# Kernel optimization log

Hardware: AMD Instinct MI355X
Metric: run time of the kernel (lower is better)

The kernel has to match this reference:

```python
import jax, jax.numpy as jnp
import numpy as np

B, NV, H, W = 4, 1, 224, 224
GH = GW = 16                 # 224 // 14 patch grid
NT = 1 + GH * GW             # 257 tokens (cls + patches)
CIN, DF, DH = 1152, 512, 128
NP0 = 512
UPF = (4, 8)
RADIUS = 1.0


def setup_inputs():
    key = jax.random.key(0)
    ks = jax.random.split(key, 8)
    rn = lambda k, s, sc: jax.random.normal(k, s) * sc
    points = jax.random.uniform(ks[0], (B, NP0, 3), minval=-0.5, maxval=0.5)
    tokens = rn(ks[1], (B, CIN, NT), 0.5)
    # OpenGL-style c2w (the forward flips cols 1:3 to OpenCV); camera at z=+2 looking at origin
    c2w = np.tile(np.eye(4, dtype=np.float32), (B, NV, 1, 1))
    c2w[..., 2, 3] = 2.0
    K = np.zeros((B, NV, 3, 3), dtype=np.float32)
    K[..., 0, 0] = 250.0; K[..., 1, 1] = 250.0
    K[..., 0, 2] = W / 2.0; K[..., 1, 2] = H / 2.0
    K[..., 2, 2] = 1.0
    return dict(
        points=points, input_image_tokens=tokens,
        c2w_cond=jnp.asarray(c2w), intrinsic_cond=jnp.asarray(K),
        w1=rn(ks[2], (2 * DF, CIN), CIN ** -0.5), b1=jnp.zeros((2 * DF,)),
        w2=rn(ks[3], (DF, 2 * DF), (2 * DF) ** -0.5), b2=jnp.zeros((DF,)),
        s0_w1=rn(ks[4], (DH, 3 + DF), (3 + DF) ** -0.5), s0_b1=jnp.zeros((DH,)),
        s0_ow=rn(ks[5], (UPF[0] * 3, DH), DH ** -0.5), s0_ob=jnp.zeros((UPF[0] * 3,)),
        s1_w1=rn(ks[6], (DH, 3 + DF), (3 + DF) ** -0.5), s1_b1=jnp.zeros((DH,)),
        s1_ow=rn(ks[7], (UPF[1] * 3, DH), DH ** -0.5), s1_ob=jnp.zeros((UPF[1] * 3,)))


def _points_projection(pts, c2w, K, lf):
    # pts: (B,N,3), c2w: (B,4,4) OpenCV, K: (B,3,3), lf: (B,C,H,W)
    N = pts.shape[1]
    w2c = jnp.linalg.inv(c2w)
    cam = jnp.einsum('bij,bnj->bni', w2c[:, :3, :3], pts) + w2c[:, None, :3, 3]
    z = cam[..., 2]
    zs = jnp.where(jnp.abs(z) > 1e-8, z, 1e-8)
    px = K[:, 0, 0][:, None] * cam[..., 0] / zs + K[:, 0, 2][:, None]
    py = K[:, 1, 1][:, None] * cam[..., 1] / zs + K[:, 1, 2][:, None]
    ix = jnp.floor(px).astype(jnp.int32)
    iy = jnp.floor(py).astype(jnp.int32)
    valid = (z > 1e-6) & (ix >= 0) & (ix < W) & (iy >= 0) & (iy < H)
    pix = jnp.where(valid, iy * W + ix, H * W)                  # (B,N); dummy bin H*W
    nseg = B * (H * W + 1)
    seg = (jnp.arange(B)[:, None] * (H * W + 1) + pix).reshape(-1)
    zf = jnp.where(valid, z, jnp.inf).reshape(-1)
    minz = jax.ops.segment_min(zf, seg, num_segments=nseg)      # z-buffer (points_per_pixel=1)
    ismin = valid.reshape(-1) & (zf <= minz[seg])
    pid = jnp.arange(B * N)
    win = jax.ops.segment_min(jnp.where(ismin, pid, B * N), seg, num_segments=nseg)
    visible = (pid == win[seg]).reshape(B, N)                   # unique winner per pixel
    lff = lf.reshape(B, -1, H * W)
    g = jnp.take_along_axis(lff, jnp.clip(pix, 0, H * W - 1)[:, None, :], axis=2)  # (B,C,N)
    return jnp.where(visible[:, None, :], g, 0.0)


def reference(points, input_image_tokens, c2w_cond, intrinsic_cond,
              w1, b1, w2, b2, s0_w1, s0_b1, s0_ow, s0_ob, s1_w1, s1_b1, s1_ow, s1_ob):
    # mlp_feat_cond: 1x1 conv MLP over tokens
    feat = jax.nn.relu(jnp.einsum('oc,bcn->bon', w1, input_image_tokens) + b1[:, None])
    feat = jnp.einsum('oc,bcn->bon', w2, feat) + b2[:, None]    # (B, DF, NT)
    # OpenGL -> OpenCV flip of c2w columns 1:3
    flip = jnp.ones((4, 4)).at[:3, 1:3].set(-1.0)
    c2w = c2w_cond[:, 0] * flip
    Kmat = intrinsic_cond[:, 0]
    # drop cls token, to patch grid, bilinear upsample to image resolution
    lf = jnp.transpose(feat, (0, 2, 1))[:, 1:].reshape(B, GH, GW, DF)
    lf = jnp.transpose(lf, (0, 3, 1, 2))
    lf = jax.image.resize(lf, (B, DF, H, W), method='bilinear')  # (B, DF, H, W)
    pts = points
    pcd = jnp.transpose(points, (0, 2, 1))                      # (B,3,N)
    stages = (((s0_w1, s0_b1, s0_ow, s0_ob), UPF[0]), ((s1_w1, s1_b1, s1_ow, s1_ob), UPF[1]))
    outs = []
    for (ws, bs, ow, ob), f in stages:
        up_cond = _points_projection(pts, c2w, Kmat, lf)        # (B, DF, N) visibility-masked gather
        h = jax.nn.relu(jnp.einsum('oc,bcn->bon', ws,
                                   jnp.concatenate([pcd, up_cond], axis=1)) + bs[:, None])
        off = jnp.tanh(jnp.einsum('oc,bcn->bon', ow, h) + ob[:, None])  # (B, 3f, N)
        n = pcd.shape[2]
        off = off.reshape(B, f, 3, n).transpose(0, 2, 3, 1).reshape(B, 3, n * f)
        pcd = jnp.repeat(pcd, f, axis=2) + off * RADIUS         # SPD-style bounded upsample
        pts = jnp.transpose(pcd, (0, 2, 1))
        outs.append(pts)
    return tuple(outs)
```

## Files before the change

kernel.cpp:

```cpp
#include <hip/hip_runtime.h>
#include <hip/hip_bf16.h>
#include <cstdint>
#include <cstddef>

using bf16 = __hip_bfloat16;
typedef __attribute__((ext_vector_type(8))) short bf16x8_t;
typedef __attribute__((ext_vector_type(4))) float f32x4_t;

#define BB 4
#define HH 224
#define WWD 224
#define NTOK 257
#define CINC 1152
#define DFC 512

constexpr size_t OFF_G2    = 256;
constexpr size_t OFF_WC    = OFF_G2;
constexpr size_t OFF_T     = OFF_G2 + 1052672;
constexpr size_t OFF_SCR   = 256 + 2105344;
constexpr size_t OFF_FEAT1 = OFF_SCR;
constexpr size_t OFF_ZBUF  = OFF_SCR;
constexpr size_t OFF_PINFO = OFF_SCR + 1605632;
constexpr size_t WS_NEED   = OFF_SCR + 1736704;
constexpr size_t WS_FULL   = OFF_SCR + 4210688;

__device__ __forceinline__ float ldf(const void* p, size_t i, bool f32) {
  return f32 ? ((const float*)p)[i] : __bfloat162float(((const bf16*)p)[i]);
}
__device__ __forceinline__ double ldd(const void* p, size_t i, bool f32) {
  return f32 ? (double)((const float*)p)[i]
             : (double)__bfloat162float(((const bf16*)p)[i]);
}
__device__ __forceinline__ bool detect_f32(const void* c2w_raw) {
  const float* fc = (const float*)c2w_raw;
  return (fc[0] == 1.0f) && (fc[5] == 1.0f);
}

__device__ void compute_cam(const void* c2w_raw, const void* K_raw, int b, bool f32,
                            double* cw) {
  double m[16];
#pragma unroll
  for (int i = 0; i < 16; ++i) m[i] = ldd(c2w_raw, b*16 + i, f32);
  m[1]=-m[1]; m[2]=-m[2]; m[5]=-m[5]; m[6]=-m[6]; m[9]=-m[9]; m[10]=-m[10];
  double i0  =  m[5]*m[10]*m[15] - m[5]*m[11]*m[14] - m[9]*m[6]*m[15] + m[9]*m[7]*m[14] + m[13]*m[6]*m[11] - m[13]*m[7]*m[10];
  double i4  = -m[4]*m[10]*m[15] + m[4]*m[11]*m[14] + m[8]*m[6]*m[15] - m[8]*m[7]*m[14] - m[12]*m[6]*m[11] + m[12]*m[7]*m[10];
  double i8  =  m[4]*m[9]*m[15]  - m[4]*m[11]*m[13] - m[8]*m[5]*m[15] + m[8]*m[7]*m[13] + m[12]*m[5]*m[11] - m[12]*m[7]*m[9];
  double i12 = -m[4]*m[9]*m[14]  + m[4]*m[10]*m[13] + m[8]*m[5]*m[14] - m[8]*m[6]*m[13] - m[12]*m[5]*m[10] + m[12]*m[6]*m[9];
  double i1  = -m[1]*m[10]*m[15] + m[1]*m[11]*m[14] + m[9]*m[2]*m[15] - m[9]*m[3]*m[14] - m[13]*m[2]*m[11] + m[13]*m[3]*m[10];
  double i5  =  m[0]*m[10]*m[15] - m[0]*m[11]*m[14] - m[8]*m[2]*m[15] + m[8]*m[3]*m[14] + m[12]*m[2]*m[11] - m[12]*m[3]*m[10];
  double i9  = -m[0]*m[9]*m[15]  + m[0]*m[11]*m[13] + m[8]*m[1]*m[15] - m[8]*m[3]*m[13] - m[12]*m[1]*m[11] + m[12]*m[3]*m[9];
  double i13 =  m[0]*m[9]*m[14]  - m[0]*m[10]*m[13] - m[8]*m[1]*m[14] + m[8]*m[2]*m[13] + m[12]*m[1]*m[10] - m[12]*m[2]*m[9];
  double i2  =  m[1]*m[6]*m[15]  - m[1]*m[7]*m[14]  - m[5]*m[2]*m[15] + m[5]*m[3]*m[14] + m[13]*m[2]*m[7]  - m[13]*m[3]*m[6];
  double i6  = -m[0]*m[6]*m[15]  + m[0]*m[7]*m[14]  + m[4]*m[2]*m[15] - m[4]*m[3]*m[14] - m[12]*m[2]*m[7]  + m[12]*m[3]*m[6];
  double i10 =  m[0]*m[5]*m[15]  - m[0]*m[7]*m[13]  - m[4]*m[1]*m[15] + m[4]*m[3]*m[13] + m[12]*m[1]*m[7]  - m[12]*m[3]*m[5];
  double i14 = -m[0]*m[5]*m[14]  + m[0]*m[6]*m[13]  + m[4]*m[1]*m[14] - m[4]*m[2]*m[13] - m[12]*m[1]*m[6]  + m[12]*m[2]*m[5];
  double i3  = -m[1]*m[6]*m[11]  + m[1]*m[7]*m[10]  + m[5]*m[2]*m[11] - m[5]*m[3]*m[10] - m[9]*m[2]*m[7]   + m[9]*m[3]*m[6];
  double i7  =  m[0]*m[6]*m[11]  - m[0]*m[7]*m[10]  - m[4]*m[2]*m[11] + m[4]*m[3]*m[10] + m[8]*m[2]*m[7]   - m[8]*m[3]*m[6];
  double i11 = -m[0]*m[5]*m[11]  + m[0]*m[7]*m[9]   + m[4]*m[1]*m[11] - m[4]*m[3]*m[9]  - m[8]*m[1]*m[7]   + m[8]*m[3]*m[5];
  double det = m[0]*i0 + m[1]*i4 + m[2]*i8 + m[3]*i12;
  double r = 1.0 / det;
  cw[0]=i0*r;  cw[1]=i1*r;  cw[2]=i2*r;  cw[3]=i3*r;
  cw[4]=i4*r;  cw[5]=i5*r;  cw[6]=i6*r;  cw[7]=i7*r;
  cw[8]=i8*r;  cw[9]=i9*r;  cw[10]=i10*r; cw[11]=i11*r;
  cw[12] = ldd(K_raw, b*9+0, f32);
  cw[13] = ldd(K_raw, b*9+2, f32);
  cw[14] = ldd(K_raw, b*9+4, f32);
  cw[15] = ldd(K_raw, b*9+5, f32);
}

template <int XK, int WK, bool TROUT, bool ATOMIC, bool BSTR, int PREC>
__global__ __launch_bounds__(256) void gemm_mfma(
    const void* __restrict__ Wm, const void* __restrict__ Wm2,
    const void* __restrict__ X, const void* __restrict__ xb,
    const float* __restrict__ bstr_p, int bstr,
    float* __restrict__ Y, const void* __restrict__ c2w_raw,
    int O, int K, int Nn, int Yld,
    int bx0, int bxm, int by0, int bym,
    int Wld, int Wc0, int skn) {
  __shared__ __align__(16) short SMEM[6 * 2560];
  short* Whi = SMEM;
  short* Wmd = SMEM + 2560;
  short* Wlo = SMEM + 5120;
  short* Xhi = SMEM + 7680;
  short* Xmd = SMEM + 10240;
  short* Xlo = SMEM + 12800;
  const bool f32 = detect_f32(c2w_raw);
  int tid = threadIdx.x;
  int n0 = blockIdx.x * 64;
  int o0 = blockIdx.y * 64;
  int bz = (int)blockIdx.z;
  int bidx = bz / skn;
  int ks = bz - bidx * skn;
  int bx = bx0 + bxm * bidx;
  int by = by0 + bym * bidx;
  int kq = K / skn;
  int kbase = ks * kq;
  int so  = tid >> 2;
  int skq = tid & 3;
  int sn  = tid & 63;
  int skg = tid >> 6;
  int wv = tid >> 6, lane = tid & 63;
  int lm = lane & 15, lq = lane >> 4;

  float wreg[8], xreg[8];
  f32x4_t acc[4] = {};

  auto load_w = [&](int c0) {
    if constexpr (WK == 3) {
      int orow = o0 + so;
      const void* Wp = (orow < 128) ? Wm : Wm2;
      size_t base = (size_t)(orow & 127) * Wld + Wc0 + c0 + skq * 8;
#pragma unroll
      for (int j = 0; j < 8; ++j) wreg[j] = ldf(Wp, base + j, f32);
    } else if constexpr (WK == 1) {
      const float* Wf = (const float*)Wm;
      size_t base = (size_t)(o0 + so) * Wld + c0 + skq * 8;
      float4 v0 = *(const float4*)(Wf + base);
      float4 v1 = *(const float4*)(Wf + base + 4);
      wreg[0]=v0.x; wreg[1]=v0.y; wreg[2]=v0.z; wreg[3]=v0.w;
      wreg[4]=v1.x; wreg[5]=v1.y; wreg[6]=v1.z; wreg[7]=v1.w;
    } else {
      size_t base = (size_t)(o0 + so) * Wld + c0 + skq * 8;
      if (f32) {
        const float* Wf = (const float*)Wm;
        float4 v0 = *(const float4*)(Wf + base);
        float4 v1 = *(const float4*)(Wf + base + 4);
        wreg[0]=v0.x; wreg[1]=v0.y; wreg[2]=v0.z; wreg[3]=v0.w;
        wreg[4]=v1.x; wreg[5]=v1.y; wreg[6]=v1.z; wreg[7]=v1.w;
      } else {
        const unsigned short* Wh = (const unsigned short*)Wm;
        ushort4 u0 = *(const ushort4*)(Wh + base);
        ushort4 u1 = *(const ushort4*)(Wh + base + 4);
        wreg[0]=__uint_as_float((unsigned)u0.x<<16); wreg[1]=__uint_as_float((unsigned)u0.y<<16);
        wreg[2]=__uint_as_float((unsigned)u0.z<<16); wreg[3]=__uint_as_float((unsigned)u0.w<<16);
        wreg[4]=__uint_as_float((unsigned)u1.x<<16); wreg[5]=__uint_as_float((unsigned)u1.y<<16);
        wreg[6]=__uint_as_float((unsigned)u1.z<<16); wreg[7]=__uint_as_float((unsigned)u1.w<<16);
      }
    }
  };
  auto load_x = [&](int c0) {
    int gn = n0 + sn;
#pragma unroll
    for (int j = 0; j < 8; ++j) {
      int c = c0 + skg * 8 + j;
      float v = 0.f;
      if (gn < Nn) {
        if (XK == 3) {
          v = (gn < 1024) ? ldf(X, (size_t)c * 1024 + gn, f32)
                          : ((gn == 1024) ? ldf(xb, c, f32) : 0.f);
        } else if (XK == 2) {
          size_t xi = ((size_t)bx * K + c) * Nn + gn;
          v = fmaxf(((const float*)X)[xi] + ldf(xb, c, f32), 0.f);
        } else {
          size_t xi = ((size_t)bx * K + c) * Nn + gn;
          v = ldf(X, xi, f32);
        }
      }
      xreg[j] = v;
    }
  };
  auto store_hi = [&](const float* r, short* hp, int off) {
    int hd[4];
#pragma unroll
    for (int d = 0; d < 4; ++d) {
      unsigned b0 = __float_as_uint(r[2*d]), b1 = __float_as_uint(r[2*d+1]);
      hd[d] = (int)((b0 >> 16) | (b1 & 0xFFFF0000u));
    }
    *(int4*)&hp[off] = make_int4(hd[0], hd[1], hd[2], hd[3]);
  };
  auto split_store3 = [&](const float* r, short* hp, short* mp, short* lp, int off) {
    int hd[4], md[4], ld[4];
#pragma unroll
    for (int d = 0; d < 4; ++d) {
      float v0 = r[2*d], v1 = r[2*d+1];
      unsigned b0 = __float_as_uint(v0), b1 = __float_as_uint(v1);
      hd[d] = (int)((b0 >> 16) | (b1 & 0xFFFF0000u));
      float h0 = __uint_as_float(b0 & 0xFFFF0000u);
      float h1 = __uint_as_float(b1 & 0xFFFF0000u);
      float r0 = v0 - h0, r1 = v1 - h1;
      unsigned c0 = __float_as_uint(r0), c1 = __float_as_uint(r1);
      md[d] = (int)((c0 >> 16) | (c1 & 0xFFFF0000u));
      float m0 = __uint_as_float(c0 & 0xFFFF0000u);
      float m1 = __uint_as_float(c1 & 0xFFFF0000u);
      unsigned e0 = __float_as_uint(r0 - m0), e1 = __float_as_uint(r1 - m1);
      ld[d] = (int)((e0 >> 16) | (e1 & 0xFFFF0000u));
    }
    *(int4*)&hp[off] = make_int4(hd[0], hd[1], hd[2], hd[3]);
    *(int4*)&mp[off] = make_int4(md[0], md[1], md[2], md[3]);
    *(int4*)&lp[off] = make_int4(ld[0], ld[1], ld[2], ld[3]);
  };

  int nkt = kq / 32;
  int woff = so * 40 + skq * 8;
  int xoff = sn * 40 + skg * 8;
  int aoff = (wv * 16 + lm) * 40 + lq * 8;
  load_w(kbase); load_x(kbase);

  if (PREC == 0 && !f32) {
    for (int kt = 0; kt < nkt; ++kt) {
      __syncthreads();
      store_hi(wreg, Whi, woff);
      store_hi(xreg, Xhi, xoff);
      __syncthreads();
      if (kt + 1 < nkt) { load_w(kbase + (kt + 1) * 32); load_x(kbase + (kt + 1) * 32); }
      bf16x8_t ahi = *(const bf16x8_t*)&Whi[aoff];
#pragma unroll
      for (int nt = 0; nt < 4; ++nt) {
        int boff = (nt * 16 + lm) * 40 + lq * 8;
        bf16x8_t bhi = *(const bf16x8_t*)&Xhi[boff];
        acc[nt] = __builtin_amdgcn_mfma_f32_16x16x32_bf16(ahi, bhi, acc[nt], 0, 0, 0);
      }
    }
  } else {
    for (int kt = 0; kt < nkt; ++kt) {
      __syncthreads();
      split_store3(wreg, Whi, Wmd, Wlo, woff);
      split_store3(xreg, Xhi, Xmd, Xlo, xoff);
      __syncthreads();
      if (kt + 1 < nkt) { load_w(kbase + (kt + 1) * 32); load_x(kbase + (kt + 1) * 32); }
      bf16x8_t ahi = *(const bf16x8_t*)&Whi[aoff];
      bf16x8_t amd = *(const bf16x8_t*)&Wmd[aoff];
      bf16x8_t alo = *(const bf16x8_t*)&Wlo[aoff];
#pragma unroll
      for (int nt = 0; nt < 4; ++nt) {
        int boff = (nt * 16 + lm) * 40 + lq * 8;
        bf16x8_t bhi = *(const bf16x8_t*)&Xhi[boff];
        bf16x8_t bmd = *(const bf16x8_t*)&Xmd[boff];
        bf16x8_t blo = *(const bf16x8_t*)&Xlo[boff];
        acc[nt] = __builtin_amdgcn_mfma_f32_16x16x32_bf16(ahi, blo, acc[nt], 0, 0, 0);
        acc[nt] = __builtin_amdgcn_mfma_f32_16x16x32_bf16(amd, bmd, acc[nt], 0, 0, 0);
        acc[nt] = __builtin_amdgcn_mfma_f32_16x16x32_bf16(alo, bhi, acc[nt], 0, 0, 0);
        acc[nt] = __builtin_amdgcn_mfma_f32_16x16x32_bf16(amd, bhi, acc[nt], 0, 0, 0);
        acc[nt] = __builtin_amdgcn_mfma_f32_16x16x32_bf16(ahi, bmd, acc[nt], 0, 0, 0);
        acc[nt] = __builtin_amdgcn_mfma_f32_16x16x32_bf16(ahi, bhi, acc[nt], 0, 0, 0);
      }
    }
  }

  if (!ATOMIC) {
#pragma unroll
    for (int nt = 0; nt < 4; ++nt) {
      int gn = n0 + nt * 16 + lm;
      if (gn < Nn) {
#pragma unroll
        for (int r = 0; r < 4; ++r) {
          int o = o0 + wv * 16 + lq * 4 + r;
          size_t yi = TROUT ? ((size_t)by * Nn + gn) * Yld + o
                            : ((size_t)by * O + o) * (size_t)Yld + gn;
          Y[yi] = acc[nt][r];
        }
      }
    }
  } else if (!TROUT) {
#pragma unroll
    for (int nt = 0; nt < 4; ++nt) {
      int gn = n0 + nt * 16 + lm;
      if (gn < Nn) {
#pragma unroll
        for (int r = 0; r < 4; ++r) {
          int o = o0 + wv * 16 + lq * 4 + r;
          float v = acc[nt][r];
          if (BSTR && ks == 0) v += bstr_p[(size_t)o * bstr];
          atomicAdd(&Y[((size_t)by * O + o) * (size_t)Yld + gn], v);
        }
      }
    }
  } else {
    __syncthreads();
    float* ts = (float*)SMEM;
#pragma unroll
    for (int nt = 0; nt < 4; ++nt) {
      int n = nt * 16 + lm;
      int ob = wv * 16 + lq * 4;
#pragma unroll
      for (int r = 0; r < 4; ++r) ts[(ob + r) * 65 + n] = acc[nt][r];
    }
    __syncthreads();
    int oo = tid & 63;
    int nb = tid >> 6;
    float bv = (BSTR && ks == 0) ? bstr_p[(size_t)(o0 + oo) * bstr] : 0.f;
#pragma unroll
    for (int i = 0; i < 16; ++i) {
      int n = nb * 16 + i;
      int gn = n0 + n;
      if (gn < Nn)
        atomicAdd(&Y[((size_t)by * Nn + gn) * (size_t)Yld + o0 + oo],
                  ts[oo * 65 + n] + bv);
    }
  }
}

template <int XK, bool RELU, bool TROUT>
__global__ __launch_bounds__(256) void gemm_k(const void* __restrict__ Wm, const void* __restrict__ X,
                                              const void* __restrict__ bias, float* __restrict__ Y,
                                              const void* __restrict__ c2w_raw, int O, int K, int Nn,
                                              int bx0, int bxm, int by0, int bym) {
  const int TK = 32;
  __shared__ __align__(16) float Ws[TK * 68];
  __shared__ __align__(16) float Xs[TK * 68];
  const bool f32 = detect_f32(c2w_raw);
  int tid = threadIdx.x;
  int n0 = blockIdx.x * 64;
  int o0 = blockIdx.y * 64;
  int bx = bx0 + bxm * (int)blockIdx.z;
  int by = by0 + bym * (int)blockIdx.z;
  int tx = tid & 15, ty = tid >> 4;
  int wo  = tid >> 3;
  int wk4 = tid & 7;
  float acc[4][4] = {};
  float4 wv[2];
  float  xv[8];

  auto load_tile = [&](int c0) {
#pragma unroll
    for (int i = 0; i < 2; ++i) {
      int o = wo + i * 32;
      size_t off = (size_t)(o0 + o) * K + c0 + 4 * wk4;
      if (f32) {
        wv[i] = *(const float4*)((const float*)Wm + off);
      } else {
        ushort4 u = *(const ushort4*)((const unsigned short*)Wm + off);
        wv[i] = make_float4(__uint_as_float((unsigned)u.x << 16),
                            __uint_as_float((unsigned)u.y << 16),
                            __uint_as_float((unsigned)u.z << 16),
                            __uint_as_float((unsigned)u.w << 16));
      }
    }
#pragma unroll
    for (int i = 0; i < 8; ++i) {
      int idx = i * 256 + tid;
      int n = idx & 63, k = idx >> 6;
      int gn = n0 + n;
      float v = 0.f;
      if (gn < Nn) {
        size_t xi = ((size_t)bx * K + c0 + k) * Nn + gn;
        v = (XK == 0) ? ldf(X, xi, f32) : ((const float*)X)[xi];
      }
      xv[i] = v;
    }
  };

  int nkt = K / TK;
  load_tile(0);
  for (int kt = 0; kt < nkt; ++kt) {
    __syncthreads();
#pragma unroll
    for (int i = 0; i < 2; ++i) {
      int o = wo + i * 32;
      Ws[(4 * wk4 + 0) * 68 + o] = wv[i].x;
      Ws[(4 * wk4 + 1) * 68 + o] = wv[i].y;
      Ws[(4 * wk4 + 2) * 68 + o] = wv[i].z;
      Ws[(4 * wk4 + 3) * 68 + o] = wv[i].w;
    }
#pragma unroll
    for (int i = 0; i < 8; ++i) {
      int idx = i * 256 + tid;
      int n = idx & 63, k = idx >> 6;
      Xs[k * 68 + n] = xv[i];
    }
    __syncthreads();
    if (kt + 1 < nkt) load_tile((kt + 1) * TK);
#pragma unroll
    for (int k = 0; k < TK; ++k) {
      const float4 a  = *(const float4*)&Ws[k * 68 + tx * 4];
      const float4 bb = *(const float4*)&Xs[k * 68 + ty * 4];
      acc[0][0] = fmaf(a.x, bb.x, acc[0][0]); acc[0][1] = fmaf(a.x, bb.y, acc[0][1]);
      acc[0][2] = fmaf(a.x, bb.z, acc[0][2]); acc[0][3] = fmaf(a.x, bb.w, acc[0][3]);
      acc[1][0] = fmaf(a.y, bb.x, acc[1][0]); acc[1][1] = fmaf(a.y, bb.y, acc[1][1]);
      acc[1][2] = fmaf(a.y, bb.z, acc[1][2]); acc[1][3] = fmaf(a.y, bb.w, acc[1][3]);
      acc[2][0] = fmaf(a.z, bb.x, acc[2][0]); acc[2][1] = fmaf(a.z, bb.y, acc[2][1]);
      acc[2][2] = fmaf(a.z, bb.z, acc[2][2]); acc[2][3] = fmaf(a.z, bb.w, acc[2][3]);
      acc[3][0] = fmaf(a.w, bb.x, acc[3][0]); acc[3][1] = fmaf(a.w, bb.y, acc[3][1]);
      acc[3][2] = fmaf(a.w, bb.z, acc[3][2]); acc[3][3] = fmaf(a.w, bb.w, acc[3][3]);
    }
  }
#pragma unroll
  for (int oi = 0; oi < 4; ++oi) {
    int o = o0 + tx * 4 + oi;
    float bv = ldf(bias, o, f32);
#pragma unroll
    for (int ni = 0; ni < 4; ++ni) {
      int gn = n0 + ty * 4 + ni;
      if (gn < Nn) {
        float v = acc[oi][ni] + bv;
        if (RELU) v = fmaxf(v, 0.f);
        size_t yi = TROUT ? ((size_t)by * Nn + gn) * O + o
                          : ((size_t)by * O + o) * Nn + gn;
        Y[yi] = v;
      }
    }
  }
}

template <int PMODE>
__global__ __launch_bounds__(256) void proj_k(const void* __restrict__ pts,
                                              const void* __restrict__ c2w_raw,
                                              const void* __restrict__ K_raw,
                                              unsigned long long* __restrict__ zbuf,
                                              int* __restrict__ pinfo, int N) {
  int m = blockIdx.x * 256 + threadIdx.x;
  if (m >= BB * N) return;
  const bool f32 = detect_f32(c2w_raw);
  int b = m / N;
  double cw[16];
  compute_cam(c2w_raw, K_raw, b, f32, cw);
  double px, py, pz;
  if (PMODE == 1) {
    const float* pf = (const float*)pts;
    px = pf[m*3+0]; py = pf[m*3+1]; pz = pf[m*3+2];
  } else {
    px = ldd(pts, (size_t)m*3+0, f32);
    py = ldd(pts, (size_t)m*3+1, f32);
    pz = ldd(pts, (size_t)m*3+2, f32);
  }
  double cx = cw[0]*px + cw[1]*py + cw[2]*pz + cw[3];
  double cy = cw[4]*px + cw[5]*py + cw[6]*pz + cw[7];
  double z  = cw[8]*px + cw[9]*py + cw[10]*pz + cw[11];
  double zs = (fabs(z) > 1e-8) ? z : 1e-8;
  double fpx = cw[12] * cx / zs + cw[13];
  double fpy = cw[14] * cy / zs + cw[15];
  double fix = floor(fpx), fiy = floor(fpy);
  bool valid = (z > 1e-6) && (fix >= 0.0) && (fix < (double)WWD) && (fiy >= 0.0) && (fiy < (double)HH);
  int* pi = pinfo + (size_t)m * 4;
  if (valid) {
    int ix = (int)fix, iy = (int)fiy;
    int zidx = b * (HH * WWD) + iy * WWD + ix;
    float zf = (float)z;
    unsigned long long key = ((unsigned long long)__float_as_uint(zf) << 32) | (unsigned)m;
    atomicMin(&zbuf[zidx], key);
    pi[0] = zidx; pi[1] = 1;
    *(unsigned long long*)(pi + 2) = key;
  } else {
    pi[0] = 0; pi[1] = 0; pi[2] = 0; pi[3] = 0;
  }
}

template <int PMODE, int F, int TM>
__global__ __launch_bounds__(256) void stage2_k(
    const void* __restrict__ pts_in,
    const float* __restrict__ Tm,
    const int* __restrict__ pinfo,
    const unsigned long long* __restrict__ zbuf,
    const void* __restrict__ w1,
    const void* __restrict__ b1,
    const void* __restrict__ ow,
    const void* __restrict__ ob,
    const void* __restrict__ c2w_raw,
    float* __restrict__ out,
    int N) {
  constexpr int TPP = 256 / TM;
  constexpr int OC  = 128 / TPP;
  __shared__ int   ro_s[TM * 4];
  __shared__ float wt_s[TM * 4];
  __shared__ float p_s[TM * 3];
  __shared__ float Wp_s[128 * 3];
  __shared__ float b1_s[128];
  __shared__ __align__(16) float ow_s[F * 3 * 132];
  __shared__ __align__(16) float Hs[TM * 132];

  const bool f32 = detect_f32(c2w_raw);
  int tid = threadIdx.x;
  int m0 = blockIdx.x * TM;

  if (tid < TM) {
    int m = m0 + tid;
    const int* pi = pinfo + (size_t)m * 4;
    int zidx = pi[0];
    unsigned long long key = *(const unsigned long long*)(pi + 2);
    bool vis = pi[1] && (zbuf[zidx] == key);
    float s = vis ? 1.f : 0.f;
    int b = m / N;
    int rem = zidx - b * (HH * WWD);
    int iy = rem / WWD, ix = rem - iy * WWD;
    float sx = fminf(fmaxf(((float)ix + 0.5f) / 14.0f - 0.5f, 0.f), 15.f);
    float sy = fminf(fmaxf(((float)iy + 0.5f) / 14.0f - 0.5f, 0.f), 15.f);
    int x0 = (int)sx, y0 = (int)sy;
    int x1 = min(x0 + 1, 15), y1 = min(y0 + 1, 15);
    float fx = sx - (float)x0, fy = sy - (float)y0;
    int base = b * NTOK;
    ro_s[tid*4+0] = (base + 1 + y0*16 + x0) * 256;
    ro_s[tid*4+1] = (base + 1 + y0*16 + x1) * 256;
    ro_s[tid*4+2] = (base + 1 + y1*16 + x0) * 256;
    ro_s[tid*4+3] = (base + 1 + y1*16 + x1) * 256;
    wt_s[tid*4+0] = s * (1.f-fy)*(1.f-fx);
    wt_s[tid*4+1] = s * (1.f-fy)*fx;
    wt_s[tid*4+2] = s * fy*(1.f-fx);
    wt_s[tid*4+3] = s * fy*fx;
#pragma unroll
    for (int d = 0; d < 3; ++d) {
      p_s[tid*3 + d] = (PMODE == 1) ? ((const float*)pts_in)[(size_t)m*3 + d]
                                    : ldf(pts_in, (size_t)m*3 + d, f32);
    }
  }
  for (int i = tid; i < 128 * 3; i += 256) Wp_s[i] = ldf(w1, (size_t)(i / 3) * 515 + (i % 3), f32);
  for (int i = tid; i < 128; i += 256) b1_s[i] = ldf(b1, i, f32);
  for (int i = tid; i < F * 3 * 128; i += 256) ow_s[(i >> 7) * 132 + (i & 127)] = ldf(ow, i, f32);
  __syncthreads();

  {
    int pt = tid / TPP;
    int tx = tid % TPP;
    int oc0 = tx * OC;
    const float* t0p = Tm + ro_s[pt*4+0] + oc0;
    const float* t1p = Tm + ro_s[pt*4+1] + oc0;
    const float* t2p = Tm + ro_s[pt*4+2] + oc0;
    const float* t3p = Tm + ro_s[pt*4+3] + oc0;
    float w0 = wt_s[pt*4+0], w1v = wt_s[pt*4+1], w2v = wt_s[pt*4+2], w3v = wt_s[pt*4+3];
    float px = p_s[pt*3+0], py = p_s[pt*3+1], pz = p_s[pt*3+2];
#pragma unroll
    for (int i = 0; i < OC; i += 4) {
      f32x4_t c0 = *(const f32x4_t*)(t0p + i);
      f32x4_t c1 = *(const f32x4_t*)(t1p + i);
      f32x4_t c2 = *(const f32x4_t*)(t2p + i);
      f32x4_t c3 = *(const f32x4_t*)(t3p + i);
      f32x4_t hv;
#pragma unroll
      for (int j = 0; j < 4; ++j) {
        int o = oc0 + i + j;
        float v = b1_s[o]
                + Wp_s[o*3+0]*px + Wp_s[o*3+1]*py + Wp_s[o*3+2]*pz
                + w0*c0[j] + w1v*c1[j] + w2v*c2[j] + w3v*c3[j];
        hv[j] = fmaxf(v, 0.f);
      }
      *(f32x4_t*)&Hs[pt * 132 + oc0 + i] = hv;
    }
  }
  __syncthreads();

  const int tasks = TM * F * 3;
  for (int t = tid; t < tasks; t += 256) {
    int mI = t % TM;
    int r  = t / TM;
    f32x4_t acc4 = {0.f, 0.f, 0.f, 0.f};
#pragma unroll
    for (int k = 0; k < 128; k += 4) {
      f32x4_t hv = *(const f32x4_t*)&Hs[mI * 132 + k];
      f32x4_t wv = *(const f32x4_t*)&ow_s[r * 132 + k];
      acc4 += hv * wv;
    }
    float dot = acc4[0] + acc4[1] + acc4[2] + acc4[3] + ldf(ob, r, f32);
    float val = tanhf(dot);
    int j = r / 3, d = r - j * 3;
    int m = m0 + mI;
    out[((size_t)m * F + j) * 3 + d] = p_s[mI * 3 + d] + val;
  }
}

template <int PMODE, int F>
__global__ __launch_bounds__(256) void stage_k(
    const void* __restrict__ pts_in,
    const float* __restrict__ g2,
    const int* __restrict__ pinfo,
    const unsigned long long* __restrict__ zbuf,
    const void* __restrict__ w1,
    const void* __restrict__ b1,
    const void* __restrict__ ow,
    const void* __restrict__ ob,
    const void* __restrict__ c2w_raw,
    float* __restrict__ out,
    int N) {
  const int TM = 16, TK = 32;
  __shared__ int   ro_s[TM * 4];
  __shared__ float wt_s[TM * 4];
  __shared__ float p_s[TM * 3];
  __shared__ float ow_s[F * 3 * 128];
  __shared__ __align__(16) float uni[4800];
  float* Ws = uni;
  float* Vs = uni + 4224;
  float* Hs = uni;

  const bool f32 = detect_f32(c2w_raw);
  int tid = threadIdx.x;
  int m0 = blockIdx.x * TM;

  if (tid < TM) {
    int m = m0 + tid;
    const int* pi = pinfo + (size_t)m * 4;
    int zidx = pi[0];
    unsigned long long key = *(const unsigned long long*)(pi + 2);
    bool vis = pi[1] && (zbuf[zidx] == key);
    float s = vis ? 1.f : 0.f;
    int b = m / N;
    int rem = zidx - b * (HH * WWD);
    int iy = rem / WWD, ix = rem - iy * WWD;
    float sx = fminf(fmaxf(((float)ix + 0.5f) / 14.0f - 0.5f, 0.f), 15.f);
    float sy = fminf(fmaxf(((float)iy + 0.5f) / 14.0f - 0.5f, 0.f), 15.f);
    int x0 = (int)sx, y0 = (int)sy;
    int x1 = min(x0 + 1, 15), y1 = min(y0 + 1, 15);
    float fx = sx - (float)x0, fy = sy - (float)y0;
    int base = b * NTOK;
    ro_s[tid*4+0] = (base + 1 + y0*16 + x0) * DFC;
    ro_s[tid*4+1] = (base + 1 + y0*16 + x1) * DFC;
    ro_s[tid*4+2] = (base + 1 + y1*16 + x0) * DFC;
    ro_s[tid*4+3] = (base + 1 + y1*16 + x1) * DFC;
    wt_s[tid*4+0] = s * (1.f-fy)*(1.f-fx);
    wt_s[tid*4+1] = s * (1.f-fy)*fx;
    wt_s[tid*4+2] = s * fy*(1.f-fx);
    wt_s[tid*4+3] = s * fy*fx;
#pragma unroll
    for (int d = 0; d < 3; ++d) {
      p_s[tid*3 + d] = (PMODE == 1) ? ((const float*)pts_in)[(size_t)m*3 + d]
                                    : ldf(pts_in, (size_t)m*3 + d, f32);
    }
  }
  for (int i = tid; i < F * 3 * 128; i += 256) ow_s[i] = ldf(ow, i, f32);
  __syncthreads();

  int tx = tid & 15, ty = tid >> 4;
  float acc[2][4] = {};
  float wreg[16];
  float greg[2][4];
  float vbase[2];

  auto prefetch = [&](int c0) {
    if (f32) {
      const float* w1f = (const float*)w1;
#pragma unroll
      for (int i = 0; i < 16; ++i) {
        int idx = i * 256 + tid;
        int k = idx & 31, o = idx >> 5;
        int c = c0 + k;
        wreg[i] = (c < 515) ? w1f[(size_t)o * 515 + c] : 0.f;
      }
    } else {
      const bf16* w1h = (const bf16*)w1;
#pragma unroll
      for (int i = 0; i < 16; ++i) {
        int idx = i * 256 + tid;
        int k = idx & 31, o = idx >> 5;
        int c = c0 + k;
        wreg[i] = (c < 515) ? __bfloat162float(w1h[(size_t)o * 515 + c]) : 0.f;
      }
    }
#pragma unroll
    for (int i = 0; i < 2; ++i) {
      int idx = i * 256 + tid;
      int mI = idx & 15, k = idx >> 4;
      int c = c0 + k;
      vbase[i] = 0.f;
      greg[i][0] = greg[i][1] = greg[i][2] = greg[i][3] = 0.f;
      if (c < 3) {
        vbase[i] = p_s[mI*3 + c];
      } else if (c < 515) {
        int ch = c - 3;
        greg[i][0] = g2[ro_s[mI*4+0] + ch];
        greg[i][1] = g2[ro_s[mI*4+1] + ch];
        greg[i][2] = g2[ro_s[mI*4+2] + ch];
        greg[i][3] = g2[ro_s[mI*4+3] + ch];
      }
    }
  };

  prefetch(0);
  for (int kt = 0; kt < 17; ++kt) {
    __syncthreads();
#pragma unroll
    for (int i = 0; i < 16; ++i) {
      int idx = i * 256 + tid;
      int k = idx & 31, o = idx >> 5;
      Ws[k * 132 + o] = wreg[i];
    }
#pragma unroll
    for (int i = 0; i < 2; ++i) {
      int idx = i * 256 + tid;
      int mI = idx & 15, k = idx >> 4;
      Vs[k * 18 + mI] = vbase[i]
        + wt_s[mI*4+0] * greg[i][0] + wt_s[mI*4+1] * greg[i][1]
        + wt_s[mI*4+2] * greg[i][2] + wt_s[mI*4+3] * greg[i][3];
    }
    __syncthreads();
    if (kt + 1 < 17) prefetch((kt + 1) * TK);
#pragma unroll
    for (int k = 0; k < TK; ++k) {
      const float4 a0 = *(const float4*)&Ws[k * 132 + tx * 4];
      const float4 a1 = *(const float4*)&Ws[k * 132 + 64 + tx * 4];
      const float  bb = Vs[k * 18 + ty];
      acc[0][0] = fmaf(a0.x, bb, acc[0][0]);
      acc[0][1] = fmaf(a0.y, bb, acc[0][1]);
      acc[0][2] = fmaf(a0.z, bb, acc[0][2]);
      acc[0][3] = fmaf(a0.w, bb, acc[0][3]);
      acc[1][0] = fmaf(a1.x, bb, acc[1][0]);
      acc[1][1] = fmaf(a1.y, bb, acc[1][1]);
      acc[1][2] = fmaf(a1.z, bb, acc[1][2]);
      acc[1][3] = fmaf(a1.w, bb, acc[1][3]);
    }
  }
  __syncthreads();
#pragma unroll
  for (int h = 0; h < 2; ++h) {
#pragma unroll
    for (int oi = 0; oi < 4; ++oi) {
      int o = h * 64 + tx * 4 + oi;
      float bv = ldf(b1, o, f32);
      Hs[o * 18 + ty] = fmaxf(acc[h][oi] + bv, 0.f);
    }
  }
  __syncthreads();
  const int tasks = TM * F * 3;
  for (int t = tid; t < tasks; t += 256) {
    int mI = t & 15, r = t >> 4;
    float dot = ldf(ob, r, f32);
#pragma unroll 8
    for (int k = 0; k < 128; ++k) dot = fmaf(ow_s[r * 128 + k], Hs[k * 18 + mI], dot);
    float val = tanhf(dot);
    int j = r / 3, d = r - j * 3;
    int m = m0 + mI;
    out[((size_t)m * F + j) * 3 + d] = p_s[mI * 3 + d] + val;
  }
}

extern "C" void kernel_launch(void* const* d_in, const int* in_sizes, int n_in,
                              void* d_out, int out_size, void* d_ws, size_t ws_size,
                              hipStream_t stream) {
  const void* points = d_in[0];
  const void* tokens = d_in[1];
  const void* c2w    = d_in[2];
  const void* intr   = d_in[3];
  const void* w1     = d_in[4];
  const void* b1     = d_in[5];
  const void* w2     = d_in[6];
  const void* b2     = d_in[7];
  const void* s0w1   = d_in[8];
  const void* s0b1   = d_in[9];
  const void* s0ow   = d_in[10];
  const void* s0ob   = d_in[11];
  const void* s1w1   = d_in[12];
  const void* s1b1   = d_in[13];
  const void* s1ow   = d_in[14];
  const void* s1ob   = d_in[15];

  if (ws_size < WS_NEED) {
    hipMemsetAsync(d_out, 0, (size_t)out_size * sizeof(float), stream);
    return;
  }

  char* ws = (char*)d_ws;
  unsigned long long* zbuf = (unsigned long long*)(ws + OFF_ZBUF);
  int* pinfo    = (int*)(ws + OFF_PINFO);
  float* out    = (float*)d_out;
  float* out0   = out;
  float* out1   = out + 24576;

  const int NB = (NTOK + 63) / 64;
  const size_t zbytes = (size_t)BB * HH * WWD * 8;

  if (ws_size >= WS_FULL) {
    float* Wc    = (float*)(ws + OFF_WC);
    float* Tb    = (float*)(ws + OFF_T);
    float* feat1 = (float*)(ws + OFF_FEAT1);

    hipMemsetAsync(ws + OFF_WC, 0, 2105344, stream);
    hipMemsetAsync(feat1, 0, 4210688, stream);

    gemm_mfma<3, 3, false, true, false, 0><<<dim3(17, 4, 4), 256, 0, stream>>>(
        s0w1, s1w1, w2, b2, nullptr, 0, Wc, c2w,
        256, 512, 1025, 1028, 0, 0, 0, 0, 515, 3, 4);

    gemm_mfma<0, 0, false, true, false, 0><<<dim3(NB, 16, 12), 256, 0, stream>>>(
        w1, nullptr, tokens, nullptr, nullptr, 0, feat1, c2w,
        1024, CINC, NTOK, NTOK, 0, 1, 0, 1, CINC, 0, 3);

    gemm_mfma<2, 1, true, true, true, 1><<<dim3(NB, 4, 32), 256, 0, stream>>>(
        Wc, nullptr, feat1, b1, Wc + 1024, 1028, Tb, c2w,
        256, 1024, NTOK, 256, 0, 1, 0, 1, 1028, 0, 8);

    hipMemsetAsync(zbuf, 0xFF, zbytes, stream);
    proj_k<0><<<(BB * 512) / 256, 256, 0, stream>>>(points, c2w, intr, zbuf, pinfo, 512);
    stage2_k<0, 4, 8><<<(BB * 512) / 8, 256, 0, stream>>>(points, Tb, pinfo, zbuf,
                                                          s0w1, s0b1, s0ow, s0ob, c2w,
                                                          out0, 512);
    hipMemsetAsync(zbuf, 0xFF, zbytes, stream);
    proj_k<1><<<(BB * 2048) / 256, 256, 0, stream>>>(out0, c2w, intr, zbuf, pinfo, 2048);
    stage2_k<1, 8, 8><<<(BB * 2048) / 8, 256, 0, stream>>>(out0, Tb + 128, pinfo, zbuf,
                                                           s1w1, s1b1, s1ow, s1ob, c2w,
                                                           out1, 2048);
  } else {
    float* g2    = (float*)(ws + OFF_G2);
    float* feat1 = (float*)(ws + OFF_FEAT1);
    for (int b = 0; b < BB; ++b) {
      gemm_k<0, true, false><<<dim3(NB, 16, 1), 256, 0, stream>>>(
          w1, tokens, b1, feat1, c2w, 1024, CINC, NTOK, b, 0, 0, 0);
      gemm_k<1, false, true><<<dim3(NB, 8, 1), 256, 0, stream>>>(
          w2, feat1, b2, g2, c2w, 512, 1024, NTOK, 0, 0, b, 0);
    }
    hipMemsetAsync(zbuf, 0xFF, zbytes, stream);
    proj_k<0><<<(BB * 512) / 256, 256, 0, stream>>>(points, c2w, intr, zbuf, pinfo, 512);
    stage_k<0, 4><<<(BB * 512) / 16, 256, 0, stream>>>(points, g2, pinfo, zbuf,
                                                       s0w1, s0b1, s0ow, s0ob, c2w,
                                                       out0, 512);
    hipMemsetAsync(zbuf, 0xFF, zbytes, stream);
    proj_k<1><<<(BB * 2048) / 256, 256, 0, stream>>>(out0, c2w, intr, zbuf, pinfo, 2048);
    stage_k<1, 8><<<(BB * 2048) / 16, 256, 0, stream>>>(out0, g2, pinfo, zbuf,
                                                        s1w1, s1b1, s1ow, s1ob, c2w,
                                                        out1, 2048);
  }
}
```

Measured before the change: 218.0 us.

## Restructure pipeline: split-K partials, fp32 second GEMM, fused stage-1 projection

The first GEMM now writes split-K partial sums to separate buffers instead of using atomics, and it skips the cls token. A new fp32 SIMT GEMM sums those partials, adds the bias and applies ReLU while loading, then computes the second projection. Stage 0 now projects its own output points into a second z-buffer, which removes a separate projection kernel. Both z-buffers are cleared with a single memset, and the feat1 memset is dropped. In exchange the workspace grows much larger, the full path is taken only when the workspace is big enough, and the second GEMM moves off MFMA to plain FMA.

```diff
diff --git a/kernel.cpp b/kernel.cpp
--- a/kernel.cpp
+++ b/kernel.cpp
@@ -14,15 +14,18 @@
 #define CINC 1152
 #define DFC 512
 
-constexpr size_t OFF_G2    = 256;
-constexpr size_t OFF_WC    = OFF_G2;
-constexpr size_t OFF_T     = OFF_G2 + 1052672;
-constexpr size_t OFF_SCR   = 256 + 2105344;
-constexpr size_t OFF_FEAT1 = OFF_SCR;
-constexpr size_t OFF_ZBUF  = OFF_SCR;
-constexpr size_t OFF_PINFO = OFF_SCR + 1605632;
-constexpr size_t WS_NEED   = OFF_SCR + 1736704;
-constexpr size_t WS_FULL   = OFF_SCR + 4210688;
+constexpr size_t OFF_WC     = 256;
+constexpr size_t OFF_T      = OFF_WC + 1052672;
+constexpr size_t OFF_FP     = OFF_T + 1048576;
+constexpr size_t OFF_ZB0    = OFF_FP + 12582912;
+constexpr size_t OFF_ZB1    = OFF_ZB0 + 1605632;
+constexpr size_t OFF_PI0    = OFF_ZB1 + 1605632;
+constexpr size_t OFF_PI1    = OFF_PI0 + 32768;
+constexpr size_t WS_FULL4   = OFF_PI1 + 131072;
+constexpr size_t OFF_SCR    = 256 + 2105344;
+constexpr size_t OFF_ZBUF   = OFF_SCR;
+constexpr size_t OFF_PINFO  = OFF_SCR + 1605632;
+constexpr size_t WS_NEED    = OFF_SCR + 1736704;
 
 __device__ __forceinline__ float ldf(const void* p, size_t i, bool f32) {
   return f32 ? ((const float*)p)[i] : __bfloat162float(((const bf16*)p)[i]);
@@ -68,13 +71,38 @@
   cw[15] = ldd(K_raw, b*9+5, f32);
 }
 
-template <int XK, int WK, bool TROUT, bool ATOMIC, bool BSTR, int PREC>
+__device__ __forceinline__ void project_point(
+    double px, double py, double pz, const double* cw, int b, int m,
+    unsigned long long* __restrict__ zbuf, int* __restrict__ pinfo) {
+  double cx = cw[0]*px + cw[1]*py + cw[2]*pz + cw[3];
+  double cy = cw[4]*px + cw[5]*py + cw[6]*pz + cw[7];
+  double z  = cw[8]*px + cw[9]*py + cw[10]*pz + cw[11];
+  double zs = (fabs(z) > 1e-8) ? z : 1e-8;
+  double fpx = cw[12] * cx / zs + cw[13];
+  double fpy = cw[14] * cy / zs + cw[15];
+  double fix = floor(fpx), fiy = floor(fpy);
+  bool valid = (z > 1e-6) && (fix >= 0.0) && (fix < (double)WWD) && (fiy >= 0.0) && (fiy < (double)HH);
+  int* pi = pinfo + (size_t)m * 4;
+  if (valid) {
+    int ix = (int)fix, iy = (int)fiy;
+    int zidx = b * (HH * WWD) + iy * WWD + ix;
+    float zf = (float)z;
+    unsigned long long key = ((unsigned long long)__float_as_uint(zf) << 32) | (unsigned)m;
+    atomicMin(&zbuf[zidx], key);
+    pi[0] = zidx; pi[1] = 1;
+    *(unsigned long long*)(pi + 2) = key;
+  } else {
+    pi[0] = 0; pi[1] = 0; pi[2] = 0; pi[3] = 0;
+  }
+}
+
+template <int XK, int WK, bool TROUT, bool ATOMIC, bool BSTR, int PREC, bool PART = false>
 __global__ __launch_bounds__(256) void gemm_mfma(
     const void* __restrict__ Wm, const void* __restrict__ Wm2,
     const void* __restrict__ X, const void* __restrict__ xb,
     const float* __restrict__ bstr_p, int bstr,
     float* __restrict__ Y, const void* __restrict__ c2w_raw,
-    int O, int K, int Nn, int Yld,
+    int O, int K, int Nn, int Yld, int Xld, int Xc0,
     int bx0, int bxm, int by0, int bym,
     int Wld, int Wc0, int skn) {
   __shared__ __align__(16) short SMEM[6 * 2560];
@@ -112,13 +140,6 @@
       size_t base = (size_t)(orow & 127) * Wld + Wc0 + c0 + skq * 8;
 #pragma unroll
       for (int j = 0; j < 8; ++j) wreg[j] = ldf(Wp, base + j, f32);
-    } else if constexpr (WK == 1) {
-      const float* Wf = (const float*)Wm;
-      size_t base = (size_t)(o0 + so) * Wld + c0 + skq * 8;
-      float4 v0 = *(const float4*)(Wf + base);
-      float4 v1 = *(const float4*)(Wf + base + 4);
-      wreg[0]=v0.x; wreg[1]=v0.y; wreg[2]=v0.z; wreg[3]=v0.w;
-      wreg[4]=v1.x; wreg[5]=v1.y; wreg[6]=v1.z; wreg[7]=v1.w;
     } else {
       size_t base = (size_t)(o0 + so) * Wld + c0 + skq * 8;
       if (f32) {
@@ -148,11 +169,8 @@
         if (XK == 3) {
           v = (gn < 1024) ? ldf(X, (size_t)c * 1024 + gn, f32)
                           : ((gn == 1024) ? ldf(xb, c, f32) : 0.f);
-        } else if (XK == 2) {
-          size_t xi = ((size_t)bx * K + c) * Nn + gn;
-          v = fmaxf(((const float*)X)[xi] + ldf(xb, c, f32), 0.f);
         } else {
-          size_t xi = ((size_t)bx * K + c) * Nn + gn;
+          size_t xi = ((size_t)bx * K + c) * Xld + Xc0 + gn;
           v = ldf(X, xi, f32);
         }
       }
@@ -237,7 +255,20 @@
     }
   }
 
-  if (!ATOMIC) {
+  if constexpr (PART) {
+    float* Yp = Y + (size_t)ks * (size_t)bstr;
+#pragma unroll
+    for (int nt = 0; nt < 4; ++nt) {
+      int gn = n0 + nt * 16 + lm;
+      if (gn < Nn) {
+#pragma unroll
+        for (int r = 0; r < 4; ++r) {
+          int o = o0 + wv * 16 + lq * 4 + r;
+          Yp[((size_t)by * O + o) * (size_t)Yld + gn] = acc[nt][r];
+        }
+      }
+    }
+  } else if (!ATOMIC) {
 #pragma unroll
     for (int nt = 0; nt < 4; ++nt) {
       int gn = n0 + nt * 16 + lm;
@@ -251,7 +282,7 @@
         }
       }
     }
-  } else if (!TROUT) {
+  } else {
 #pragma unroll
     for (int nt = 0; nt < 4; ++nt) {
       int gn = n0 + nt * 16 + lm;
@@ -265,28 +296,101 @@
         }
       }
     }
-  } else {
+  }
+}
+
+template <int SK>
+__global__ __launch_bounds__(256) void tgemm_k(
+    const float* __restrict__ Wc,
+    const float* __restrict__ fp,
+    const void* __restrict__ b1,
+    float* __restrict__ T,
+    const void* __restrict__ c2w_raw) {
+  const int TK = 32;
+  const int PS = BB * 1024 * 256;
+  __shared__ __align__(16) float uni[64 * 68];
+  float* Ws = uni;
+  float* Xs = uni + TK * 68;
+  const bool f32 = detect_f32(c2w_raw);
+  int tid = threadIdx.x;
+  int n0 = blockIdx.x * 64;
+  int o0 = blockIdx.y * 64;
+  int bz = (int)blockIdx.z;
+  int b  = bz / SK;
+  int ks = bz - b * SK;
+  const int kq = 1024 / SK;
+  int kbase = ks * kq;
+  int tx = tid & 15, ty = tid >> 4;
+  int wo = tid >> 3, wk4 = tid & 7;
+  float acc[4][4] = {};
+  float4 wv[2];
+  float xv[8];
+
+  auto load_tile = [&](int c0) {
+#pragma unroll
+    for (int i = 0; i < 2; ++i) {
+      int o = o0 + wo + i * 32;
+      wv[i] = *(const float4*)(Wc + (size_t)o * 1028 + kbase + c0 + 4 * wk4);
+    }
+#pragma unroll
+    for (int i = 0; i < 8; ++i) {
+      int idx = i * 256 + tid;
+      int n = idx & 63, k = idx >> 6;
+      int kk = kbase + c0 + k;
+      size_t xi = ((size_t)b * 1024 + kk) * 256 + n0 + n;
+      float v = fp[xi] + fp[PS + xi] + fp[2 * PS + xi] + ldf(b1, kk, f32);
+      xv[i] = fmaxf(v, 0.f);
+    }
+  };
+
+  int nkt = kq / TK;
+  load_tile(0);
+  for (int kt = 0; kt < nkt; ++kt) {
     __syncthreads();
-    float* ts = (float*)SMEM;
-#pragma unroll
-    for (int nt = 0; nt < 4; ++nt) {
-      int n = nt * 16 + lm;
-      int ob = wv * 16 + lq * 4;
-#pragma unroll
-      for (int r = 0; r < 4; ++r) ts[(ob + r) * 65 + n] = acc[nt][r];
+#pragma unroll
+    for (int i = 0; i < 2; ++i) {
+      int o = wo + i * 32;
+      Ws[(4 * wk4 + 0) * 68 + o] = wv[i].x;
+      Ws[(4 * wk4 + 1) * 68 + o] = wv[i].y;
+      Ws[(4 * wk4 + 2) * 68 + o] = wv[i].z;
+      Ws[(4 * wk4 + 3) * 68 + o] = wv[i].w;
+    }
+#pragma unroll
+    for (int i = 0; i < 8; ++i) {
+      int idx = i * 256 + tid;
+      int n = idx & 63, k = idx >> 6;
+      Xs[k * 68 + n] = xv[i];
     }
     __syncthreads();
-    int oo = tid & 63;
-    int nb = tid >> 6;
-    float bv = (BSTR && ks == 0) ? bstr_p[(size_t)(o0 + oo) * bstr] : 0.f;
-#pragma unroll
-    for (int i = 0; i < 16; ++i) {
-      int n = nb * 16 + i;
-      int gn = n0 + n;
-      if (gn < Nn)
-        atomicAdd(&Y[((size_t)by * Nn + gn) * (size_t)Yld + o0 + oo],
-                  ts[oo * 65 + n] + bv);
-    }
+    if (kt + 1 < nkt) load_tile((kt + 1) * TK);
+#pragma unroll
+    for (int k = 0; k < TK; ++k) {
+      const float4 a  = *(const float4*)&Ws[k * 68 + tx * 4];
+      const float4 bb = *(const float4*)&Xs[k * 68 + ty * 4];
+      acc[0][0] = fmaf(a.x, bb.x, acc[0][0]); acc[0][1] = fmaf(a.x, bb.y, acc[0][1]);
+      acc[0][2] = fmaf(a.x, bb.z, acc[0][2]); acc[0][3] = fmaf(a.x, bb.w, acc[0][3]);
+      acc[1][0] = fmaf(a.y, bb.x, acc[1][0]); acc[1][1] = fmaf(a.y, bb.y, acc[1][1]);
+      acc[1][2] = fmaf(a.y, bb.z, acc[1][2]); acc[1][3] = fmaf(a.y, bb.w, acc[1][3]);
+      acc[2][0] = fmaf(a.z, bb.x, acc[2][0]); acc[2][1] = fmaf(a.z, bb.y, acc[2][1]);
+      acc[2][2] = fmaf(a.z, bb.z, acc[2][2]); acc[2][3] = fmaf(a.z, bb.w, acc[2][3]);
+      acc[3][0] = fmaf(a.w, bb.x, acc[3][0]); acc[3][1] = fmaf(a.w, bb.y, acc[3][1]);
+      acc[3][2] = fmaf(a.w, bb.z, acc[3][2]); acc[3][3] = fmaf(a.w, bb.w, acc[3][3]);
+    }
+  }
+  __syncthreads();
+  float* ts = uni;
+#pragma unroll
+  for (int oi = 0; oi < 4; ++oi)
+#pragma unroll
+    for (int ni = 0; ni < 4; ++ni)
+      ts[(tx * 4 + oi) * 65 + ty * 4 + ni] = acc[oi][ni];
+  __syncthreads();
+  int oo = tid & 63, nb = tid >> 6;
+  float bv = (ks == 0) ? Wc[(size_t)(o0 + oo) * 1028 + 1024] : 0.f;
+#pragma unroll
+  for (int i = 0; i < 16; ++i) {
+    int n = nb * 16 + i;
+    atomicAdd(&T[((size_t)b * 256 + n0 + n) * 256 + o0 + oo], ts[oo * 65 + n] + bv);
   }
 }
 
@@ -413,29 +517,10 @@
     py = ldd(pts, (size_t)m*3+1, f32);
     pz = ldd(pts, (size_t)m*3+2, f32);
   }
-  double cx = cw[0]*px + cw[1]*py + cw[2]*pz + cw[3];
-  double cy = cw[4]*px + cw[5]*py + cw[6]*pz + cw[7];
-  double z  = cw[8]*px + cw[9]*py + cw[10]*pz + cw[11];
-  double zs = (fabs(z) > 1e-8) ? z : 1e-8;
-  double fpx = cw[12] * cx / zs + cw[13];
-  double fpy = cw[14] * cy / zs + cw[15];
-  double fix = floor(fpx), fiy = floor(fpy);
-  bool valid = (z > 1e-6) && (fix >= 0.0) && (fix < (double)WWD) && (fiy >= 0.0) && (fiy < (double)HH);
-  int* pi = pinfo + (size_t)m * 4;
-  if (valid) {
-    int ix = (int)fix, iy = (int)fiy;
-    int zidx = b * (HH * WWD) + iy * WWD + ix;
-    float zf = (float)z;
-    unsigned long long key = ((unsigned long long)__float_as_uint(zf) << 32) | (unsigned)m;
-    atomicMin(&zbuf[zidx], key);
-    pi[0] = zidx; pi[1] = 1;
-    *(unsigned long long*)(pi + 2) = key;
-  } else {
-    pi[0] = 0; pi[1] = 0; pi[2] = 0; pi[3] = 0;
-  }
-}
-
-template <int PMODE, int F, int TM>
+  project_point(px, py, pz, cw, b, m, zbuf, pinfo);
+}
+
+template <int PMODE, int F, int TM, bool PROJ>
 __global__ __launch_bounds__(256) void stage2_k(
     const void* __restrict__ pts_in,
     const float* __restrict__ Tm,
@@ -446,6 +531,9 @@
     const void* __restrict__ ow,
     const void* __restrict__ ob,
     const void* __restrict__ c2w_raw,
+    const void* __restrict__ K_raw,
+    unsigned long long* __restrict__ zb_out,
+    int* __restrict__ pinfo_out,
     float* __restrict__ out,
     int N) {
   constexpr int TPP = 256 / TM;
@@ -455,6 +543,7 @@
   __shared__ float p_s[TM * 3];
   __shared__ float Wp_s[128 * 3];
   __shared__ float b1_s[128];
+  __shared__ float op_s[TM * F * 3];
   __shared__ __align__(16) float ow_s[F * 3 * 132];
   __shared__ __align__(16) float Hs[TM * 132];
 
@@ -477,11 +566,11 @@
     int x0 = (int)sx, y0 = (int)sy;
     int x1 = min(x0 + 1, 15), y1 = min(y0 + 1, 15);
     float fx = sx - (float)x0, fy = sy - (float)y0;
-    int base = b * NTOK;
-    ro_s[tid*4+0] = (base + 1 + y0*16 + x0) * 256;
-    ro_s[tid*4+1] = (base + 1 + y0*16 + x1) * 256;
-    ro_s[tid*4+2] = (base + 1 + y1*16 + x0) * 256;
-    ro_s[tid*4+3] = (base + 1 + y1*16 + x1) * 256;
+    int base = b * 256;
+    ro_s[tid*4+0] = (base + y0*16 + x0) * 256;
+    ro_s[tid*4+1] = (base + y0*16 + x1) * 256;
+    ro_s[tid*4+2] = (base + y1*16 + x0) * 256;
+    ro_s[tid*4+3] = (base + y1*16 + x1) * 256;
     wt_s[tid*4+0] = s * (1.f-fy)*(1.f-fx);
     wt_s[tid*4+1] = s * (1.f-fy)*fx;
     wt_s[tid*4+2] = s * fy*(1.f-fx);
@@ -542,7 +631,23 @@
     float val = tanhf(dot);
     int j = r / 3, d = r - j * 3;
     int m = m0 + mI;
-    out[((size_t)m * F + j) * 3 + d] = p_s[mI * 3 + d] + val;
+    float ov = p_s[mI * 3 + d] + val;
+    out[((size_t)m * F + j) * 3 + d] = ov;
+    if (PROJ) op_s[(mI * F + j) * 3 + d] = ov;
+  }
+
+  if constexpr (PROJ) {
+    __syncthreads();
+    if (tid < TM * F) {
+      int mo = m0 * F + tid;
+      int b = mo / (N * F);
+      double cw[16];
+      compute_cam(c2w_raw, K_raw, b, f32, cw);
+      double px = (double)op_s[tid*3+0];
+      double py = (double)op_s[tid*3+1];
+      double pz = (double)op_s[tid*3+2];
+      project_point(px, py, pz, cw, b, mo, zb_out, pinfo_out);
+    }
   }
 }
 
@@ -735,8 +840,6 @@
   }
 
   char* ws = (char*)d_ws;
-  unsigned long long* zbuf = (unsigned long long*)(ws + OFF_ZBUF);
-  int* pinfo    = (int*)(ws + OFF_PINFO);
   float* out    = (float*)d_out;
   float* out0   = out;
   float* out1   = out + 24576;
@@ -744,39 +847,41 @@
   const int NB = (NTOK + 63) / 64;
   const size_t zbytes = (size_t)BB * HH * WWD * 8;
 
-  if (ws_size >= WS_FULL) {
-    float* Wc    = (float*)(ws + OFF_WC);
-    float* Tb    = (float*)(ws + OFF_T);
-    float* feat1 = (float*)(ws + OFF_FEAT1);
-
-    hipMemsetAsync(ws + OFF_WC, 0, 2105344, stream);
-    hipMemsetAsync(feat1, 0, 4210688, stream);
+  if (ws_size >= WS_FULL4) {
+    float* Wc   = (float*)(ws + OFF_WC);
+    float* Tb   = (float*)(ws + OFF_T);
+    float* fp   = (float*)(ws + OFF_FP);
+    unsigned long long* zb0 = (unsigned long long*)(ws + OFF_ZB0);
+    unsigned long long* zb1 = (unsigned long long*)(ws + OFF_ZB1);
+    int* pinfo0 = (int*)(ws + OFF_PI0);
+    int* pinfo1 = (int*)(ws + OFF_PI1);
+
+    hipMemsetAsync(ws + OFF_WC, 0, 2101248, stream);
+    hipMemsetAsync(ws + OFF_ZB0, 0xFF, 2 * zbytes, stream);
 
     gemm_mfma<3, 3, false, true, false, 0><<<dim3(17, 4, 4), 256, 0, stream>>>(
         s0w1, s1w1, w2, b2, nullptr, 0, Wc, c2w,
-        256, 512, 1025, 1028, 0, 0, 0, 0, 515, 3, 4);
-
-    gemm_mfma<0, 0, false, true, false, 0><<<dim3(NB, 16, 12), 256, 0, stream>>>(
-        w1, nullptr, tokens, nullptr, nullptr, 0, feat1, c2w,
-        1024, CINC, NTOK, NTOK, 0, 1, 0, 1, CINC, 0, 3);
-
-    gemm_mfma<2, 1, true, true, true, 1><<<dim3(NB, 4, 32), 256, 0, stream>>>(
-        Wc, nullptr, feat1, b1, Wc + 1024, 1028, Tb, c2w,
-        256, 1024, NTOK, 256, 0, 1, 0, 1, 1028, 0, 8);
-
-    hipMemsetAsync(zbuf, 0xFF, zbytes, stream);
-    proj_k<0><<<(BB * 512) / 256, 256, 0, stream>>>(points, c2w, intr, zbuf, pinfo, 512);
-    stage2_k<0, 4, 8><<<(BB * 512) / 8, 256, 0, stream>>>(points, Tb, pinfo, zbuf,
-                                                          s0w1, s0b1, s0ow, s0ob, c2w,
-                                                          out0, 512);
-    hipMemsetAsync(zbuf, 0xFF, zbytes, stream);
-    proj_k<1><<<(BB * 2048) / 256, 256, 0, stream>>>(out0, c2w, intr, zbuf, pinfo, 2048);
-    stage2_k<1, 8, 8><<<(BB * 2048) / 8, 256, 0, stream>>>(out0, Tb + 128, pinfo, zbuf,
-                                                           s1w1, s1b1, s1ow, s1ob, c2w,
-                                                           out1, 2048);
+        256, 512, 1025, 1028, 1025, 0, 0, 0, 0, 0, 515, 3, 4);
+
+    gemm_mfma<0, 0, false, false, false, 0, true><<<dim3(4, 16, 12), 256, 0, stream>>>(
+        w1, nullptr, tokens, nullptr, nullptr,  1048576, fp, c2w,
+        1024, CINC, 256, 256, 257, 1, 0, 1, 0, 1, CINC, 0, 3);
+
+    proj_k<0><<<(BB * 512) / 256, 256, 0, stream>>>(points, c2w, intr, zb0, pinfo0, 512);
+
+    tgemm_k<4><<<dim3(4, 4, 16), 256, 0, stream>>>(Wc, fp, b1, Tb, c2w);
+
+    stage2_k<0, 4, 8, true><<<(BB * 512) / 8, 256, 0, stream>>>(
+        points, Tb, pinfo0, zb0, s0w1, s0b1, s0ow, s0ob, c2w, intr,
+        zb1, pinfo1, out0, 512);
+    stage2_k<1, 8, 8, false><<<(BB * 2048) / 8, 256, 0, stream>>>(
+        out0, Tb + 128, pinfo1, zb1, s1w1, s1b1, s1ow, s1ob, c2w, intr,
+        nullptr, nullptr, out1, 2048);
   } else {
-    float* g2    = (float*)(ws + OFF_G2);
-    float* feat1 = (float*)(ws + OFF_FEAT1);
+    float* g2    = (float*)(ws + 256);
+    float* feat1 = (float*)(ws + OFF_SCR);
+    unsigned long long* zbuf = (unsigned long long*)(ws + OFF_ZBUF);
+    int* pinfo = (int*)(ws + OFF_PINFO);
     for (int b = 0; b < BB; ++b) {
       gemm_k<0, true, false><<<dim3(NB, 16, 1), 256, 0, stream>>>(
           w1, tokens, b1, feat1, c2w, 1024, CINC, NTOK, b, 0, 0, 0);
```

Result: faster. 193.1 us (-11.4%).
